# Optimization experiments

Measured on AMD Instinct MI355X. Metric: run time of the kernel, lower is better.

Reference implementation:

```python
import jax, jax.numpy as jnp
import numpy as np

B, N, D = 4, 2048, 1024
H, HD = 16, 64
MAX_SEQ = 4096
INNER = H * HD


def setup_inputs() -> dict:
    key = jax.random.key(0)
    ks = jax.random.split(key, 5)
    s = 0.02
    return {
        "x": jax.random.normal(ks[0], (B, N, D), dtype=jnp.float32),
        "ln_gamma": jnp.ones((D,), jnp.float32),
        "ln_beta": jnp.zeros((D,), jnp.float32),
        "w_qkv": jax.random.normal(ks[1], (D, 3 * INNER), dtype=jnp.float32) * s,
        "w_out": jax.random.normal(ks[2], (INNER, D), dtype=jnp.float32) * s,
        "b_out": jnp.zeros((D,), jnp.float32),
    }


def _rope_tables(n, head_dim):
    inv_freq = 1.0 / (10000.0 ** (jnp.arange(0, head_dim, 2, dtype=jnp.float32) / head_dim))
    pos = jnp.arange(n, dtype=jnp.float32)
    ang = pos[:, None] * inv_freq[None, :]  # [n, hd/2]
    return jnp.sin(ang), jnp.cos(ang)


def reference(x, ln_gamma, ln_beta, w_qkv, w_out, b_out):
    b, n, d = x.shape
    # LayerNorm
    mu = jnp.mean(x, axis=-1, keepdims=True)
    var = jnp.var(x, axis=-1, keepdims=True)
    xn = (x - mu) / jnp.sqrt(var + 1e-5) * ln_gamma + ln_beta
    # QKV projection (no bias)
    qkv = xn @ w_qkv  # [b, n, 3*inner]
    q, k, v = jnp.split(qkv, 3, axis=-1)
    def to_heads(t):
        return t.reshape(b, n, H, HD).transpose(0, 2, 1, 3)  # b h n d
    q, k, v = to_heads(q), to_heads(k), to_heads(v)
    # RoPE (half-split rotation, as in source)
    sin, cos = _rope_tables(n, HD)  # [n, hd/2]
    sin = sin[None, None]
    cos = cos[None, None]
    half = HD // 2
    def rotate(t):
        t1, t2 = t[..., :half], t[..., half:]
        return jnp.concatenate([t1 * cos - t2 * sin, t2 * cos + t1 * sin], axis=-1)
    qr, kr = rotate(q), rotate(k)
    scale = HD ** -0.5
    scores = jnp.einsum('bhid,bhjd->bhij', qr, kr) * scale
    probs = jax.nn.softmax(scores, axis=-1)
    out = jnp.einsum('bhij,bhjd->bhid', probs, v)
    out = out.transpose(0, 2, 1, 3).reshape(b, n, INNER)
    return out @ w_out + b_out
```

## Files before the change

### kernel.cpp

```cpp
#include <hip/hip_runtime.h>
#include <hip/hip_bf16.h>

#define Bb   4
#define Nn   2048
#define Dd   1024
#define Hh   16
#define HDd  64
#define IN3  3072
#define RR   8192


typedef __attribute__((ext_vector_type(8))) short short8;
typedef __attribute__((ext_vector_type(4))) float floatx4;

#define MFMA16(a, b, c) __builtin_amdgcn_mfma_f32_16x16x32_bf16((a), (b), (c), 0, 0, 0)

static __device__ __forceinline__ unsigned short f2bf(float f) {
    union { float f; unsigned int u; } v; v.f = f;
    unsigned int r = v.u + 0x7fffu + ((v.u >> 16) & 1u);
    return (unsigned short)(r >> 16);
}
static __device__ __forceinline__ float bf2f(unsigned short h) {
    union { unsigned int u; float f; } v; v.u = ((unsigned int)h) << 16;
    return v.f;
}

static __device__ __forceinline__ float fast_exp2(float x) {
#if __has_builtin(__builtin_amdgcn_exp2f)
    return __builtin_amdgcn_exp2f(x);
#else
    return exp2f(x);
#endif
}

static __device__ __forceinline__ void sincos_rev(float ang, float& s, float& c) {
#if __has_builtin(__builtin_amdgcn_sinf) && __has_builtin(__builtin_amdgcn_cosf)
    float rev = ang * 0.15915494309189535f;
    rev = rev - floorf(rev);
    s = __builtin_amdgcn_sinf(rev);
    c = __builtin_amdgcn_cosf(rev);
#else
    s = sinf(ang);
    c = cosf(ang);
#endif
}

typedef const __attribute__((address_space(1))) void* gas1_t;
typedef __attribute__((address_space(3))) void* las3_t;
static __device__ __forceinline__ void load_lds16(const void* g, void* l) {
    __builtin_amdgcn_global_load_lds((gas1_t)(unsigned long long)g,
                                     (las3_t)(unsigned int)(unsigned long long)l,
                                     16, 0, 0);
}

__global__ __launch_bounds__(256) void prep_kernel(const float* __restrict__ wqkv,
                                                   unsigned short* __restrict__ wqkvT,
                                                   const float* __restrict__ wout,
                                                   unsigned short* __restrict__ woutT,
                                                   const float* __restrict__ x,
                                                   const float* __restrict__ g,
                                                   const float* __restrict__ be,
                                                   unsigned short* __restrict__ xn) {
    __shared__ float smem[32 * 33];
    int bid = blockIdx.x;
    if (bid < 4096) {
        const float* src; unsigned short* dst; int cols, c0, r0;
        if (bid < 3072) { src = wqkv; dst = wqkvT; cols = 3072; c0 = (bid % 96) * 32; r0 = (bid / 96) * 32; }
        else { int b2 = bid - 3072; src = wout; dst = woutT; cols = 1024; c0 = (b2 & 31) * 32; r0 = (b2 >> 5) * 32; }
        int tx = threadIdx.x & 31, ty = threadIdx.x >> 5;
#pragma unroll
        for (int i = 0; i < 4; ++i) smem[(ty + 8 * i) * 33 + tx] = src[(r0 + ty + 8 * i) * cols + c0 + tx];
        __syncthreads();
#pragma unroll
        for (int i = 0; i < 4; ++i) dst[(c0 + ty + 8 * i) * 1024 + r0 + tx] = f2bf(smem[tx * 33 + ty + 8 * i]);
        return;
    }
    int row = bid - 4096, t = threadIdx.x;
    float4 v = ((const float4*)(x + row * Dd))[t];
    float s  = v.x + v.y + v.z + v.w;
    float sq = v.x * v.x + v.y * v.y + v.z * v.z + v.w * v.w;
#pragma unroll
    for (int off = 1; off < 64; off <<= 1) { s += __shfl_xor(s, off); sq += __shfl_xor(sq, off); }
    float* ps = smem; float* pq2 = smem + 4;
    int wv = t >> 6;
    if ((t & 63) == 0) { ps[wv] = s; pq2[wv] = sq; }
    __syncthreads();
    s  = ps[0] + ps[1] + ps[2] + ps[3];
    sq = pq2[0] + pq2[1] + pq2[2] + pq2[3];
    float mu   = s * (1.0f / Dd);
    float var  = sq * (1.0f / Dd) - mu * mu;
    float rstd = rsqrtf(var + 1e-5f);
    float4 gg = ((const float4*)g)[t];
    float4 bb = ((const float4*)be)[t];
    ushort4 o;
    o.x = f2bf((v.x - mu) * rstd * gg.x + bb.x);
    o.y = f2bf((v.y - mu) * rstd * gg.y + bb.y);
    o.z = f2bf((v.z - mu) * rstd * gg.z + bb.z);
    o.w = f2bf((v.w - mu) * rstd * gg.w + bb.w);
    ((ushort4*)(xn + row * Dd))[t] = o;
}

__global__ __launch_bounds__(512, 1) void gemm_qkv(const unsigned short* __restrict__ A,
                                                   const unsigned short* __restrict__ Bt,
                                                   unsigned short* __restrict__ qo,
                                                   unsigned short* __restrict__ ko,
                                                   unsigned short* __restrict__ vo) {
    __shared__ unsigned short LDS[49152];
    int r0 = blockIdx.x * 128, c0 = blockIdx.y * 256;
    int tid = threadIdx.x;
    int wv = tid >> 6, lane = tid & 63, l15 = lane & 15, quad = lane >> 4;
    int wm = wv >> 2, wn = wv & 3;

    floatx4 acc[4][4] = {};
    int swz0 = (quad ^ (l15 & 7)) << 3;
    int swz1 = ((4 | quad) ^ (l15 & 7)) << 3;

    auto stageA = [&](int tt) {
        unsigned short* base = &LDS[(tt & 1) * 8192];
        int k0 = tt * 64;
#pragma unroll
        for (int i = 0; i < 2; ++i) {
            int qq = (wv * 2 + i) * 64 + lane;
            int row = qq >> 3, cp = qq & 7;
            int sc = cp ^ (row & 7);
            load_lds16(&A[(r0 + row) * 1024 + k0 + sc * 8], &base[qq * 8]);
        }
    };
    auto stageB = [&](int tt) {
        unsigned short* base = &LDS[16384 + (tt & 1) * 16384];
        int k0 = tt * 64;
#pragma unroll
        for (int i = 0; i < 4; ++i) {
            int qq = (wv * 4 + i) * 64 + lane;
            int row = qq >> 3, cp = qq & 7;
            int sc = cp ^ (row & 7);
            load_lds16(&Bt[(c0 + row) * 1024 + k0 + sc * 8], &base[qq * 8]);
        }
    };

    stageA(0); stageB(0); stageA(1);
    asm volatile("s_waitcnt vmcnt(2)" ::: "memory");
    __builtin_amdgcn_s_barrier();

    for (int t = 0; t < 16; ++t) {
        int abuf = (t & 1) * 8192;
        int bbuf = 16384 + (t & 1) * 16384;
        short8 af[4][2], bf[2][2];

        if (t < 15) stageB(t + 1);
#pragma unroll
        for (int mi = 0; mi < 4; ++mi) {
            af[mi][0] = *(const short8*)&LDS[abuf + (wm * 64 + mi * 16 + l15) * 64 + swz0];
            af[mi][1] = *(const short8*)&LDS[abuf + (wm * 64 + mi * 16 + l15) * 64 + swz1];
        }
#pragma unroll
        for (int ni = 0; ni < 2; ++ni) {
            bf[ni][0] = *(const short8*)&LDS[bbuf + (wn * 64 + ni * 16 + l15) * 64 + swz0];
            bf[ni][1] = *(const short8*)&LDS[bbuf + (wn * 64 + ni * 16 + l15) * 64 + swz1];
        }
        __builtin_amdgcn_s_barrier();
        asm volatile("s_waitcnt lgkmcnt(0)" ::: "memory");
        __builtin_amdgcn_s_setprio(1);
#pragma unroll
        for (int ks = 0; ks < 2; ++ks)
#pragma unroll
            for (int mi = 0; mi < 4; ++mi)
#pragma unroll
                for (int ni = 0; ni < 2; ++ni)
                    acc[mi][ni] = MFMA16(af[mi][ks], bf[ni][ks], acc[mi][ni]);
        __builtin_amdgcn_s_setprio(0);
        __builtin_amdgcn_s_barrier();

        if (t < 14) stageA(t + 2);
#pragma unroll
        for (int ni = 0; ni < 2; ++ni) {
            bf[ni][0] = *(const short8*)&LDS[bbuf + (wn * 64 + 32 + ni * 16 + l15) * 64 + swz0];
            bf[ni][1] = *(const short8*)&LDS[bbuf + (wn * 64 + 32 + ni * 16 + l15) * 64 + swz1];
        }
        __builtin_amdgcn_s_barrier();
        asm volatile("s_waitcnt lgkmcnt(0)" ::: "memory");
        __builtin_amdgcn_s_setprio(1);
#pragma unroll
        for (int ks = 0; ks < 2; ++ks)
#pragma unroll
            for (int mi = 0; mi < 4; ++mi)
#pragma unroll
                for (int ni = 0; ni < 2; ++ni)
                    acc[mi][2 + ni] = MFMA16(af[mi][ks], bf[ni][ks], acc[mi][2 + ni]);
        __builtin_amdgcn_s_setprio(0);
        if (t < 14)       asm volatile("s_waitcnt vmcnt(2)" ::: "memory");
        else if (t == 14) asm volatile("s_waitcnt vmcnt(0)" ::: "memory");
        __builtin_amdgcn_s_barrier();
    }

    if (c0 >= 2048) {
        unsigned short* T2 = LDS;
#pragma unroll
        for (int mi = 0; mi < 4; ++mi)
#pragma unroll
            for (int ni = 0; ni < 4; ++ni) {
                ushort4 w4;
                w4.x = f2bf(acc[mi][ni][0]);
                w4.y = f2bf(acc[mi][ni][1]);
                w4.z = f2bf(acc[mi][ni][2]);
                w4.w = f2bf(acc[mi][ni][3]);
                int col = wn * 64 + ni * 16 + l15;
                int row = wm * 64 + mi * 16 + quad * 4;
                *(ushort4*)&T2[col * 136 + row] = w4;
            }
        __syncthreads();
        int col = tid >> 1, seg = tid & 1;
        int hglob = ((c0 - 2048) >> 6) + (col >> 6);
        int j = col & 63;
        int b = r0 >> 11;
        int n0g = (r0 & 2047) + seg * 64;
        unsigned short tmp[64];
#pragma unroll
        for (int gi = 0; gi < 16; ++gi) {
            int blk = seg * 2 + (gi >> 3);
            int srow = blk * 32 + 16 * (gi & 1) + 4 * ((gi >> 1) & 3);
            *(ushort4*)&tmp[gi * 4] = *(const ushort4*)&T2[col * 136 + srow];
        }
        unsigned short* dst = vo + (((long)(b * 16 + hglob)) * 64 + j) * 2048 + n0g;
#pragma unroll
        for (int k2 = 0; k2 < 8; ++k2)
            *(short8*)(dst + k2 * 8) = *(const short8*)&tmp[k2 * 8];
        return;
    }

    {
        const float crope = 13.287712379549449f / 32.0f;
        float invf0 = fast_exp2(-(float)l15 * crope);
        float invf1 = fast_exp2(-(float)(l15 + 16) * crope);
#pragma unroll
        for (int mi = 0; mi < 4; ++mi)
#pragma unroll
            for (int r2 = 0; r2 < 4; ++r2) {
                int rr = r0 + wm * 64 + mi * 16 + quad * 4 + r2;
                float n = (float)(rr & 2047);
                float s0, c0r, s1, c1r;
                sincos_rev(n * invf0, s0, c0r);
                sincos_rev(n * invf1, s1, c1r);
                float t1a = acc[mi][0][r2], t2a = acc[mi][2][r2];
                acc[mi][0][r2] = t1a * c0r - t2a * s0;
                acc[mi][2][r2] = t2a * c0r + t1a * s0;
                float t1b = acc[mi][1][r2], t2b = acc[mi][3][r2];
                acc[mi][1][r2] = t1b * c1r - t2b * s1;
                acc[mi][3][r2] = t2b * c1r + t1b * s1;
            }
    }
    if (c0 < 1024) {
        const float qsc = 0.125f * 1.4426950408889634f;
#pragma unroll
        for (int mi = 0; mi < 4; ++mi)
#pragma unroll
            for (int ni = 0; ni < 4; ++ni)
#pragma unroll
                for (int r2 = 0; r2 < 4; ++r2) acc[mi][ni][r2] *= qsc;
    }
    unsigned short* outp = (c0 < 1024) ? qo : ko;
#pragma unroll
    for (int ni = 0; ni < 4; ++ni) {
        int c = c0 + wn * 64 + ni * 16 + l15;
        int cin = c & 1023;
        int h = cin >> 6, j = cin & 63;
#pragma unroll
        for (int mi = 0; mi < 4; ++mi) {
#pragma unroll
            for (int r2 = 0; r2 < 4; ++r2) {
                int rr = r0 + wm * 64 + mi * 16 + quad * 4 + r2;
                int b = rr >> 11, n = rr & 2047;
                int bh = b * 16 + h;
                outp[(bh * 2048 + n) * 64 + j] = f2bf(acc[mi][ni][r2]);
            }
        }
    }
}

__global__ __launch_bounds__(256, 3) void attn_kernel(const unsigned short* __restrict__ q,
                                                      const unsigned short* __restrict__ k,
                                                      const unsigned short* __restrict__ vt,
                                                      unsigned short* __restrict__ attn) {
    __shared__ unsigned short KVs[3][2][64 * 64];
    int fid = blockIdx.x;
    int xcd = fid & 7, rest = fid >> 3;
    int qi = rest & 15, bhg = rest >> 4;
    int bh = bhg * 8 + xcd;
    int q0 = qi * 128;
    int tid = threadIdx.x;
    int wave = tid >> 6, lane = tid & 63, l15 = lane & 15, quad = lane >> 4;
    const unsigned short* qb  = q  + bh * (Nn * HDd);
    const unsigned short* kbp = k  + bh * (Nn * HDd);
    const unsigned short* vb  = vt + bh * (HDd * Nn);
    int qbase = q0 + wave * 32;

    short8 bq[2][2];
#pragma unroll
    for (int g = 0; g < 2; ++g) {
        bq[g][0] = *(const short8*)&qb[(qbase + g * 16 + l15) * 64 + quad * 8];
        bq[g][1] = *(const short8*)&qb[(qbase + g * 16 + l15) * 64 + 32 + quad * 8];
    }

    auto stage = [&](int buf, int kb0) {
#pragma unroll
        for (int i = 0; i < 2; ++i) {
            int c = wave * 2 + i;
            int p = c * 64 + lane;
            int row = p >> 3, pr = p & 7;
            int sc = pr ^ (row & 7);
            load_lds16(&kbp[(kb0 + row) * 64 + sc * 8], &KVs[buf][0][p * 8]);
            load_lds16(&vb[row * Nn + kb0 + sc * 8],    &KVs[buf][1][p * 8]);
        }
    };

    floatx4 ot[2][4] = {};
    floatx4 osum[2] = {};
    const floatx4 fz = {0.0f, 0.0f, 0.0f, 0.0f};
    const short8 vones = {(short)0x3F80, (short)0x3F80, (short)0x3F80, (short)0x3F80,
                          (short)0x3F80, (short)0x3F80, (short)0x3F80, (short)0x3F80};
    int swz0 = (quad ^ (l15 & 7)) << 3;
    int swz1 = ((4 | quad) ^ (l15 & 7)) << 3;

    auto body = [&](int cur, int nxt, int kt) {
        if (kt + 2 < 32) stage(nxt, (kt + 2) * 64);
        const unsigned short* Kc = KVs[cur][0];
        const unsigned short* Vc = KVs[cur][1];
        short8 ka0[4], ka1[4];
#pragma unroll
        for (int mb = 0; mb < 4; ++mb) {
            ka0[mb] = *(const short8*)&Kc[(mb * 16 + l15) * 64 + swz0];
            ka1[mb] = *(const short8*)&Kc[(mb * 16 + l15) * 64 + swz1];
        }
        short8 bv0[4], bv1[4];
#pragma unroll
        for (int ht = 0; ht < 4; ++ht) {
            int row = (ht * 16 + l15) * 64;
            bv0[ht] = *(const short8*)&Vc[row + swz0];
            bv1[ht] = *(const short8*)&Vc[row + swz1];
        }
#pragma unroll
        for (int g = 0; g < 2; ++g) {
            floatx4 st[4];
            __builtin_amdgcn_s_setprio(1);
#pragma unroll
            for (int mb = 0; mb < 4; ++mb) {
                floatx4 z = MFMA16(ka0[mb], bq[g][0], fz);
                st[mb] = MFMA16(ka1[mb], bq[g][1], z);
            }
            __builtin_amdgcn_s_setprio(0);
            short8 pa[2];
#pragma unroll
            for (int c = 0; c < 2; ++c) {
                union { ushort4 u[2]; short8 s; } w;
#pragma unroll
                for (int t2 = 0; t2 < 2; ++t2) {
                    int mb = 2 * c + t2;
                    float p0 = fast_exp2(st[mb][0]);
                    float p1 = fast_exp2(st[mb][1]);
                    float p2 = fast_exp2(st[mb][2]);
                    float p3 = fast_exp2(st[mb][3]);
                    *(__hip_bfloat162*)&w.u[t2].x = __float22bfloat162_rn(float2{p0, p1});
                    *(__hip_bfloat162*)&w.u[t2].z = __float22bfloat162_rn(float2{p2, p3});
                }
                pa[c] = w.s;
            }
            __builtin_amdgcn_s_setprio(1);
            osum[g] = MFMA16(pa[0], vones, osum[g]);
            osum[g] = MFMA16(pa[1], vones, osum[g]);
#pragma unroll
            for (int ht = 0; ht < 4; ++ht) {
                ot[g][ht] = MFMA16(pa[0], bv0[ht], ot[g][ht]);
                ot[g][ht] = MFMA16(pa[1], bv1[ht], ot[g][ht]);
            }
            __builtin_amdgcn_s_setprio(0);
        }
        if (kt < 30)       asm volatile("s_waitcnt vmcnt(4)" ::: "memory");
        else if (kt == 30) asm volatile("s_waitcnt vmcnt(0)" ::: "memory");
        __builtin_amdgcn_s_barrier();
    };

    stage(0, 0);
    stage(1, 64);
    asm volatile("s_waitcnt vmcnt(4)" ::: "memory");
    __builtin_amdgcn_s_barrier();
    for (int kt = 0; kt < 30; kt += 3) {
        body(0, 2, kt);
        body(1, 0, kt + 1);
        body(2, 1, kt + 2);
    }
    body(0, 2, 30);
    body(1, 0, 31);

    int b = bh >> 4, h = bh & 15;
    unsigned short* ob = ((unsigned short*)KVs) + wave * 1152;
#pragma unroll
    for (int g = 0; g < 2; ++g) {
        float il[4];
#pragma unroll
        for (int r = 0; r < 4; ++r) il[r] = 1.0f / osum[g][r];
#pragma unroll
        for (int ht = 0; ht < 4; ++ht)
#pragma unroll
            for (int r = 0; r < 4; ++r)
                ob[(quad * 4 + r) * 72 + ht * 16 + l15] = f2bf(ot[g][ht][r] * il[r]);
        int q_loc = lane >> 2, seg = lane & 3;
        unsigned short* dst = attn + ((long)(b * Nn + q0 + wave * 32 + g * 16 + q_loc)) * 1024 + h * 64 + seg * 16;
        *(short8*)dst       = *(const short8*)&ob[q_loc * 72 + seg * 16];
        *(short8*)(dst + 8) = *(const short8*)&ob[q_loc * 72 + seg * 16 + 8];
    }
}

__global__ __launch_bounds__(512, 1) void gemm_out(const unsigned short* __restrict__ A,
                                                   const unsigned short* __restrict__ Bt,
                                                   const float* __restrict__ bout,
                                                   float* __restrict__ out) {
    __shared__ unsigned short LDS[49152];
    int r0 = blockIdx.x * 128, c0 = blockIdx.y * 256;
    int tid = threadIdx.x;
    int wv = tid >> 6, lane = tid & 63, l15 = lane & 15, quad = lane >> 4;
    int wm = wv >> 2, wn = wv & 3;

    floatx4 acc[4][4] = {};
    int swz0 = (quad ^ (l15 & 7)) << 3;
    int swz1 = ((4 | quad) ^ (l15 & 7)) << 3;

    auto stageA = [&](int tt) {
        unsigned short* base = &LDS[(tt & 1) * 8192];
        int k0 = tt * 64;
#pragma unroll
        for (int i = 0; i < 2; ++i) {
            int qq = (wv * 2 + i) * 64 + lane;
            int row = qq >> 3, cp = qq & 7;
            int sc = cp ^ (row & 7);
            load_lds16(&A[(r0 + row) * 1024 + k0 + sc * 8], &base[qq * 8]);
        }
    };
    auto stageB = [&](int tt) {
        unsigned short* base = &LDS[16384 + (tt & 1) * 16384];
        int k0 = tt * 64;
#pragma unroll
        for (int i = 0; i < 4; ++i) {
            int qq = (wv * 4 + i) * 64 + lane;
            int row = qq >> 3, cp = qq & 7;
            int sc = cp ^ (row & 7);
            load_lds16(&Bt[(c0 + row) * 1024 + k0 + sc * 8], &base[qq * 8]);
        }
    };

    stageA(0); stageB(0); stageA(1);
    asm volatile("s_waitcnt vmcnt(2)" ::: "memory");
    __builtin_amdgcn_s_barrier();

    for (int t = 0; t < 16; ++t) {
        int abuf = (t & 1) * 8192;
        int bbuf = 16384 + (t & 1) * 16384;
        short8 af[4][2], bf[2][2];

        if (t < 15) stageB(t + 1);
#pragma unroll
        for (int mi = 0; mi < 4; ++mi) {
            af[mi][0] = *(const short8*)&LDS[abuf + (wm * 64 + mi * 16 + l15) * 64 + swz0];
            af[mi][1] = *(const short8*)&LDS[abuf + (wm * 64 + mi * 16 + l15) * 64 + swz1];
        }
#pragma unroll
        for (int ni = 0; ni < 2; ++ni) {
            bf[ni][0] = *(const short8*)&LDS[bbuf + (wn * 64 + ni * 16 + l15) * 64 + swz0];
            bf[ni][1] = *(const short8*)&LDS[bbuf + (wn * 64 + ni * 16 + l15) * 64 + swz1];
        }
        __builtin_amdgcn_s_barrier();
        asm volatile("s_waitcnt lgkmcnt(0)" ::: "memory");
        __builtin_amdgcn_s_setprio(1);
#pragma unroll
        for (int ks = 0; ks < 2; ++ks)
#pragma unroll
            for (int mi = 0; mi < 4; ++mi)
#pragma unroll
                for (int ni = 0; ni < 2; ++ni)
                    acc[mi][ni] = MFMA16(af[mi][ks], bf[ni][ks], acc[mi][ni]);
        __builtin_amdgcn_s_setprio(0);
        __builtin_amdgcn_s_barrier();

        if (t < 14) stageA(t + 2);
#pragma unroll
        for (int ni = 0; ni < 2; ++ni) {
            bf[ni][0] = *(const short8*)&LDS[bbuf + (wn * 64 + 32 + ni * 16 + l15) * 64 + swz0];
            bf[ni][1] = *(const short8*)&LDS[bbuf + (wn * 64 + 32 + ni * 16 + l15) * 64 + swz1];
        }
        __builtin_amdgcn_s_barrier();
        asm volatile("s_waitcnt lgkmcnt(0)" ::: "memory");
        __builtin_amdgcn_s_setprio(1);
#pragma unroll
        for (int ks = 0; ks < 2; ++ks)
#pragma unroll
            for (int mi = 0; mi < 4; ++mi)
#pragma unroll
                for (int ni = 0; ni < 2; ++ni)
                    acc[mi][2 + ni] = MFMA16(af[mi][ks], bf[ni][ks], acc[mi][2 + ni]);
        __builtin_amdgcn_s_setprio(0);
        if (t < 14)       asm volatile("s_waitcnt vmcnt(2)" ::: "memory");
        else if (t == 14) asm volatile("s_waitcnt vmcnt(0)" ::: "memory");
        __builtin_amdgcn_s_barrier();
    }

#pragma unroll
    for (int ni = 0; ni < 4; ++ni) {
        int c = c0 + wn * 64 + ni * 16 + l15;
        float bias = bout[c];
#pragma unroll
        for (int mi = 0; mi < 4; ++mi)
#pragma unroll
            for (int r2 = 0; r2 < 4; ++r2) {
                int rr = r0 + wm * 64 + mi * 16 + quad * 4 + r2;
                out[rr * 1024 + c] = acc[mi][ni][r2] + bias;
            }
    }
}

extern "C" void kernel_launch(void* const* d_in, const int* in_sizes, int n_in,
                              void* d_out, int out_size, void* d_ws, size_t ws_size,
                              hipStream_t stream) {
    const float* x    = (const float*)d_in[0];
    const float* g    = (const float*)d_in[1];
    const float* be   = (const float*)d_in[2];
    const float* wqkv = (const float*)d_in[3];
    const float* wout = (const float*)d_in[4];
    const float* bout = (const float*)d_in[5];
    float* out = (float*)d_out;

    char* ws = (char*)d_ws;
    unsigned short* xn    = (unsigned short*)(ws);
    unsigned short* wqkvT = (unsigned short*)(ws + 16777216);
    unsigned short* woutT = (unsigned short*)(ws + 23068672);
    unsigned short* qb    = (unsigned short*)(ws + 25165824);
    unsigned short* kb    = (unsigned short*)(ws + 41943040);
    unsigned short* vt    = (unsigned short*)(ws + 58720256);
    unsigned short* attn  = (unsigned short*)(ws + 75497472);

    prep_kernel<<<4096 + RR, 256, 0, stream>>>(wqkv, wqkvT, wout, woutT, x, g, be, xn);
    gemm_qkv<<<dim3(RR / 128, IN3 / 256), 512, 0, stream>>>(xn, wqkvT, qb, kb, vt);
    attn_kernel<<<dim3(Nn / 128 * Bb * Hh), 256, 0, stream>>>(qb, kb, vt, attn);
    gemm_out<<<dim3(RR / 128, Dd / 256), 512, 0, stream>>>(attn, woutT, bout, out);
}
```

Before: 257.5 us.

## Fuse Q, K, V column tiles into one persistent block per QKV GEMM workgroup

Each QKV GEMM workgroup now computes three 256-column tiles (Q, K, V at the same offset) in sequence, looping over 48 K-steps and running the Q and K epilogues in the middle of the loop. The grid drops from 12 to 4 column blocks. Because the A operand is re-staged from global memory for each tile, the intent is mainly to cut launch and tail effects and to keep the pipeline continuous across tiles. The cost is fewer workgroups (256), which may underfill the GPU's CUs, and no overlap of loads during the mid-loop epilogues.

After: 361.9 us. +40.5%, slower.

```diff
diff --git a/kernel.cpp b/kernel.cpp
--- a/kernel.cpp
+++ b/kernel.cpp
@@ -106,18 +106,19 @@
                                                    unsigned short* __restrict__ ko,
                                                    unsigned short* __restrict__ vo) {
     __shared__ unsigned short LDS[49152];
-    int r0 = blockIdx.x * 128, c0 = blockIdx.y * 256;
+    int r0 = blockIdx.x * 128, c0base = blockIdx.y * 256;
     int tid = threadIdx.x;
     int wv = tid >> 6, lane = tid & 63, l15 = lane & 15, quad = lane >> 4;
     int wm = wv >> 2, wn = wv & 3;
 
     floatx4 acc[4][4] = {};
+    const floatx4 fz = {0.0f, 0.0f, 0.0f, 0.0f};
     int swz0 = (quad ^ (l15 & 7)) << 3;
     int swz1 = ((4 | quad) ^ (l15 & 7)) << 3;
 
-    auto stageA = [&](int tt) {
-        unsigned short* base = &LDS[(tt & 1) * 8192];
-        int k0 = tt * 64;
+    auto stageA = [&](int u2) {
+        unsigned short* base = &LDS[(u2 & 1) * 8192];
+        int k0 = (u2 & 15) * 64;
 #pragma unroll
         for (int i = 0; i < 2; ++i) {
             int qq = (wv * 2 + i) * 64 + lane;
@@ -126,9 +127,10 @@
             load_lds16(&A[(r0 + row) * 1024 + k0 + sc * 8], &base[qq * 8]);
         }
     };
-    auto stageB = [&](int tt) {
-        unsigned short* base = &LDS[16384 + (tt & 1) * 16384];
-        int k0 = tt * 64;
+    auto stageB = [&](int u1) {
+        unsigned short* base = &LDS[16384 + (u1 & 1) * 16384];
+        int c0 = c0base + (u1 >> 4) * 1024;
+        int k0 = (u1 & 15) * 64;
 #pragma unroll
         for (int i = 0; i < 4; ++i) {
             int qq = (wv * 4 + i) * 64 + lane;
@@ -138,97 +140,7 @@
         }
     };
 
-    stageA(0); stageB(0); stageA(1);
-    asm volatile("s_waitcnt vmcnt(2)" ::: "memory");
-    __builtin_amdgcn_s_barrier();
-
-    for (int t = 0; t < 16; ++t) {
-        int abuf = (t & 1) * 8192;
-        int bbuf = 16384 + (t & 1) * 16384;
-        short8 af[4][2], bf[2][2];
-
-        if (t < 15) stageB(t + 1);
-#pragma unroll
-        for (int mi = 0; mi < 4; ++mi) {
-            af[mi][0] = *(const short8*)&LDS[abuf + (wm * 64 + mi * 16 + l15) * 64 + swz0];
-            af[mi][1] = *(const short8*)&LDS[abuf + (wm * 64 + mi * 16 + l15) * 64 + swz1];
-        }
-#pragma unroll
-        for (int ni = 0; ni < 2; ++ni) {
-            bf[ni][0] = *(const short8*)&LDS[bbuf + (wn * 64 + ni * 16 + l15) * 64 + swz0];
-            bf[ni][1] = *(const short8*)&LDS[bbuf + (wn * 64 + ni * 16 + l15) * 64 + swz1];
-        }
-        __builtin_amdgcn_s_barrier();
-        asm volatile("s_waitcnt lgkmcnt(0)" ::: "memory");
-        __builtin_amdgcn_s_setprio(1);
-#pragma unroll
-        for (int ks = 0; ks < 2; ++ks)
-#pragma unroll
-            for (int mi = 0; mi < 4; ++mi)
-#pragma unroll
-                for (int ni = 0; ni < 2; ++ni)
-                    acc[mi][ni] = MFMA16(af[mi][ks], bf[ni][ks], acc[mi][ni]);
-        __builtin_amdgcn_s_setprio(0);
-        __builtin_amdgcn_s_barrier();
-
-        if (t < 14) stageA(t + 2);
-#pragma unroll
-        for (int ni = 0; ni < 2; ++ni) {
-            bf[ni][0] = *(const short8*)&LDS[bbuf + (wn * 64 + 32 + ni * 16 + l15) * 64 + swz0];
-            bf[ni][1] = *(const short8*)&LDS[bbuf + (wn * 64 + 32 + ni * 16 + l15) * 64 + swz1];
-        }
-        __builtin_amdgcn_s_barrier();
-        asm volatile("s_waitcnt lgkmcnt(0)" ::: "memory");
-        __builtin_amdgcn_s_setprio(1);
-#pragma unroll
-        for (int ks = 0; ks < 2; ++ks)
-#pragma unroll
-            for (int mi = 0; mi < 4; ++mi)
-#pragma unroll
-                for (int ni = 0; ni < 2; ++ni)
-                    acc[mi][2 + ni] = MFMA16(af[mi][ks], bf[ni][ks], acc[mi][2 + ni]);
-        __builtin_amdgcn_s_setprio(0);
-        if (t < 14)       asm volatile("s_waitcnt vmcnt(2)" ::: "memory");
-        else if (t == 14) asm volatile("s_waitcnt vmcnt(0)" ::: "memory");
-        __builtin_amdgcn_s_barrier();
-    }
-
-    if (c0 >= 2048) {
-        unsigned short* T2 = LDS;
-#pragma unroll
-        for (int mi = 0; mi < 4; ++mi)
-#pragma unroll
-            for (int ni = 0; ni < 4; ++ni) {
-                ushort4 w4;
-                w4.x = f2bf(acc[mi][ni][0]);
-                w4.y = f2bf(acc[mi][ni][1]);
-                w4.z = f2bf(acc[mi][ni][2]);
-                w4.w = f2bf(acc[mi][ni][3]);
-                int col = wn * 64 + ni * 16 + l15;
-                int row = wm * 64 + mi * 16 + quad * 4;
-                *(ushort4*)&T2[col * 136 + row] = w4;
-            }
-        __syncthreads();
-        int col = tid >> 1, seg = tid & 1;
-        int hglob = ((c0 - 2048) >> 6) + (col >> 6);
-        int j = col & 63;
-        int b = r0 >> 11;
-        int n0g = (r0 & 2047) + seg * 64;
-        unsigned short tmp[64];
-#pragma unroll
-        for (int gi = 0; gi < 16; ++gi) {
-            int blk = seg * 2 + (gi >> 3);
-            int srow = blk * 32 + 16 * (gi & 1) + 4 * ((gi >> 1) & 3);
-            *(ushort4*)&tmp[gi * 4] = *(const ushort4*)&T2[col * 136 + srow];
-        }
-        unsigned short* dst = vo + (((long)(b * 16 + hglob)) * 64 + j) * 2048 + n0g;
-#pragma unroll
-        for (int k2 = 0; k2 < 8; ++k2)
-            *(short8*)(dst + k2 * 8) = *(const short8*)&tmp[k2 * 8];
-        return;
-    }
-
-    {
+    auto epilogue_qk = [&](int job) {
         const float crope = 13.287712379549449f / 32.0f;
         float invf0 = fast_exp2(-(float)l15 * crope);
         float invf1 = fast_exp2(-(float)(l15 + 16) * crope);
@@ -248,32 +160,129 @@
                 acc[mi][1][r2] = t1b * c1r - t2b * s1;
                 acc[mi][3][r2] = t2b * c1r + t1b * s1;
             }
-    }
-    if (c0 < 1024) {
-        const float qsc = 0.125f * 1.4426950408889634f;
+        if (job == 0) {
+            const float qsc = 0.125f * 1.4426950408889634f;
+#pragma unroll
+            for (int mi = 0; mi < 4; ++mi)
+#pragma unroll
+                for (int ni = 0; ni < 4; ++ni)
+#pragma unroll
+                    for (int r2 = 0; r2 < 4; ++r2) acc[mi][ni][r2] *= qsc;
+        }
+        unsigned short* outp = (job == 0) ? qo : ko;
+        int c0 = c0base + job * 1024;
+#pragma unroll
+        for (int ni = 0; ni < 4; ++ni) {
+            int c = c0 + wn * 64 + ni * 16 + l15;
+            int cin = c & 1023;
+            int h = cin >> 6, j = cin & 63;
+#pragma unroll
+            for (int mi = 0; mi < 4; ++mi) {
+#pragma unroll
+                for (int r2 = 0; r2 < 4; ++r2) {
+                    int rr = r0 + wm * 64 + mi * 16 + quad * 4 + r2;
+                    int b = rr >> 11, n = rr & 2047;
+                    int bh = b * 16 + h;
+                    outp[(bh * 2048 + n) * 64 + j] = f2bf(acc[mi][ni][r2]);
+                }
+            }
+        }
 #pragma unroll
         for (int mi = 0; mi < 4; ++mi)
 #pragma unroll
-            for (int ni = 0; ni < 4; ++ni)
-#pragma unroll
-                for (int r2 = 0; r2 < 4; ++r2) acc[mi][ni][r2] *= qsc;
-    }
-    unsigned short* outp = (c0 < 1024) ? qo : ko;
-#pragma unroll
-    for (int ni = 0; ni < 4; ++ni) {
-        int c = c0 + wn * 64 + ni * 16 + l15;
-        int cin = c & 1023;
-        int h = cin >> 6, j = cin & 63;
+            for (int ni = 0; ni < 4; ++ni) acc[mi][ni] = fz;
+    };
+
+    stageA(0); stageB(0); stageA(1);
+    asm volatile("s_waitcnt vmcnt(2)" ::: "memory");
+    __builtin_amdgcn_s_barrier();
+
+    for (int u = 0; u < 48; ++u) {
+        int abuf = (u & 1) * 8192;
+        int bbuf = 16384 + (u & 1) * 16384;
+        short8 af[4][2], bf[2][2];
+
+        if (u < 47) stageB(u + 1);
 #pragma unroll
         for (int mi = 0; mi < 4; ++mi) {
-#pragma unroll
-            for (int r2 = 0; r2 < 4; ++r2) {
-                int rr = r0 + wm * 64 + mi * 16 + quad * 4 + r2;
-                int b = rr >> 11, n = rr & 2047;
-                int bh = b * 16 + h;
-                outp[(bh * 2048 + n) * 64 + j] = f2bf(acc[mi][ni][r2]);
-            }
-        }
+            af[mi][0] = *(const short8*)&LDS[abuf + (wm * 64 + mi * 16 + l15) * 64 + swz0];
+            af[mi][1] = *(const short8*)&LDS[abuf + (wm * 64 + mi * 16 + l15) * 64 + swz1];
+        }
+#pragma unroll
+        for (int ni = 0; ni < 2; ++ni) {
+            bf[ni][0] = *(const short8*)&LDS[bbuf + (wn * 64 + ni * 16 + l15) * 64 + swz0];
+            bf[ni][1] = *(const short8*)&LDS[bbuf + (wn * 64 + ni * 16 + l15) * 64 + swz1];
+        }
+        __builtin_amdgcn_s_barrier();
+        asm volatile("s_waitcnt lgkmcnt(0)" ::: "memory");
+        __builtin_amdgcn_s_setprio(1);
+#pragma unroll
+        for (int ks = 0; ks < 2; ++ks)
+#pragma unroll
+            for (int mi = 0; mi < 4; ++mi)
+#pragma unroll
+                for (int ni = 0; ni < 2; ++ni)
+                    acc[mi][ni] = MFMA16(af[mi][ks], bf[ni][ks], acc[mi][ni]);
+        __builtin_amdgcn_s_setprio(0);
+        __builtin_amdgcn_s_barrier();
+
+        if (u < 46) stageA(u + 2);
+#pragma unroll
+        for (int ni = 0; ni < 2; ++ni) {
+            bf[ni][0] = *(const short8*)&LDS[bbuf + (wn * 64 + 32 + ni * 16 + l15) * 64 + swz0];
+            bf[ni][1] = *(const short8*)&LDS[bbuf + (wn * 64 + 32 + ni * 16 + l15) * 64 + swz1];
+        }
+        __builtin_amdgcn_s_barrier();
+        asm volatile("s_waitcnt lgkmcnt(0)" ::: "memory");
+        __builtin_amdgcn_s_setprio(1);
+#pragma unroll
+        for (int ks = 0; ks < 2; ++ks)
+#pragma unroll
+            for (int mi = 0; mi < 4; ++mi)
+#pragma unroll
+                for (int ni = 0; ni < 2; ++ni)
+                    acc[mi][2 + ni] = MFMA16(af[mi][ks], bf[ni][ks], acc[mi][2 + ni]);
+        __builtin_amdgcn_s_setprio(0);
+        if (u < 46)       asm volatile("s_waitcnt vmcnt(2)" ::: "memory");
+        else if (u == 46) asm volatile("s_waitcnt vmcnt(0)" ::: "memory");
+        __builtin_amdgcn_s_barrier();
+
+        if (u == 15)      epilogue_qk(0);
+        else if (u == 31) epilogue_qk(1);
+    }
+
+    {
+        unsigned short* T2 = LDS;
+#pragma unroll
+        for (int mi = 0; mi < 4; ++mi)
+#pragma unroll
+            for (int ni = 0; ni < 4; ++ni) {
+                ushort4 w4;
+                w4.x = f2bf(acc[mi][ni][0]);
+                w4.y = f2bf(acc[mi][ni][1]);
+                w4.z = f2bf(acc[mi][ni][2]);
+                w4.w = f2bf(acc[mi][ni][3]);
+                int col = wn * 64 + ni * 16 + l15;
+                int row = wm * 64 + mi * 16 + quad * 4;
+                *(ushort4*)&T2[col * 136 + row] = w4;
+            }
+        __syncthreads();
+        int col = tid >> 1, seg = tid & 1;
+        int hglob = (c0base >> 6) + (col >> 6);
+        int j = col & 63;
+        int b = r0 >> 11;
+        int n0g = (r0 & 2047) + seg * 64;
+        unsigned short tmp[64];
+#pragma unroll
+        for (int gi = 0; gi < 16; ++gi) {
+            int blk = seg * 2 + (gi >> 3);
+            int srow = blk * 32 + 16 * (gi & 1) + 4 * ((gi >> 1) & 3);
+            *(ushort4*)&tmp[gi * 4] = *(const ushort4*)&T2[col * 136 + srow];
+        }
+        unsigned short* dst = vo + (((long)(b * 16 + hglob)) * 64 + j) * 2048 + n0g;
+#pragma unroll
+        for (int k2 = 0; k2 < 8; ++k2)
+            *(short8*)(dst + k2 * 8) = *(const short8*)&tmp[k2 * 8];
     }
 }
 
@@ -537,7 +546,7 @@
     unsigned short* attn  = (unsigned short*)(ws + 75497472);
 
     prep_kernel<<<4096 + RR, 256, 0, stream>>>(wqkv, wqkvT, wout, woutT, x, g, be, xn);
-    gemm_qkv<<<dim3(RR / 128, IN3 / 256), 512, 0, stream>>>(xn, wqkvT, qb, kb, vt);
+    gemm_qkv<<<dim3(RR / 128, 4), 512, 0, stream>>>(xn, wqkvT, qb, kb, vt);
     attn_kernel<<<dim3(Nn / 128 * Bb * Hh), 256, 0, stream>>>(qb, kb, vt, attn);
     gemm_out<<<dim3(RR / 128, Dd / 256), 512, 0, stream>>>(attn, woutT, bout, out);
 }
```
